# Kernel tuning notes

Measured on AMD Instinct MI355X. Metric: run time of the kernel, lower is better.

Reference implementation:

```python
import jax, jax.numpy as jnp
import numpy as np


def setup_inputs() -> dict:
    key = jax.random.key(0)
    ks = jax.random.split(key, 4)
    B, N, D, C = 8, 32768, 128, 64
    H = D // 2
    features = jax.random.normal(ks[0], (B, N, D), dtype=jnp.float32)
    cluster_assignments = jax.random.randint(ks[1], (B, N), 0, C)
    W1 = jax.random.normal(ks[2], (D, H), dtype=jnp.float32) * (1.0 / np.sqrt(D))
    b1 = jnp.zeros((H,), dtype=jnp.float32)
    W2 = jax.random.normal(ks[3], (H, 1), dtype=jnp.float32) * (1.0 / np.sqrt(H))
    b2 = jnp.zeros((1,), dtype=jnp.float32)
    return {"features": features, "cluster_assignments": cluster_assignments,
            "W1": W1, "b1": b1, "W2": W2, "b2": b2, "num_clusters": C}


def reference(features, cluster_assignments, W1, b1, W2, b2, num_clusters):
    # features: [B, N, D]; cluster_assignments: [B, N] ints in [0, num_clusters)
    B, N, D = features.shape
    # importance_net: Linear -> ReLU -> Linear -> Sigmoid
    h = jax.nn.relu(jnp.einsum('bnd,dh->bnh', features, W1) + b1)
    imp = jax.nn.sigmoid(jnp.einsum('bnh,ho->bno', h, W2) + b2)[..., 0]  # [B, N]

    # Fused per-(batch, cluster) softmax-weighted segment sum.
    num_seg = B * num_clusters
    seg = (cluster_assignments + num_clusters * jnp.arange(B)[:, None]).reshape(-1)  # [B*N]
    imp_f = imp.reshape(-1)
    # stable softmax within each segment
    seg_max = jax.ops.segment_max(imp_f, seg, num_segments=num_seg)  # -inf for empty
    e = jnp.exp(imp_f - seg_max[seg])
    denom = jax.ops.segment_sum(e, seg, num_segments=num_seg)
    w = e / denom[seg]  # [B*N]
    out = jax.ops.segment_sum(features.reshape(-1, D) * w[:, None], seg,
                              num_segments=num_seg)  # empty clusters -> zeros
    return out.reshape(B, num_clusters, D)
```

## Files before the change

### kernel.cpp

```cpp
#include <hip/hip_runtime.h>
#include <hip/hip_bf16.h>


#define B_ 8
#define N_ 32768
#define D_ 128
#define C_ 64
#define H_ 64

#define NTHREADS 512
#define NWAVES 8
#define ROWS_PER_BLOCK 512
#define NBLOCKS ((B_ * N_) / ROWS_PER_BLOCK)
#define SLICES (NBLOCKS / B_)
#define NSS 4
#define RST 152
#define W1S 136

typedef float f32x4 __attribute__((ext_vector_type(4)));
typedef short s16x8 __attribute__((ext_vector_type(8)));

__device__ __forceinline__ short bf16rne(float x) {
    unsigned u = __float_as_uint(x);
    u = (u + 0x7FFFu + ((u >> 16) & 1u)) >> 16;
    return (short)u;
}

__device__ __forceinline__ s16x8 pk8(float4 a, float4 b) {
    union { s16x8 v; __hip_bfloat162 h[4]; } u;
    u.h[0] = __float22bfloat162_rn(make_float2(a.x, a.y));
    u.h[1] = __float22bfloat162_rn(make_float2(a.z, a.w));
    u.h[2] = __float22bfloat162_rn(make_float2(b.x, b.y));
    u.h[3] = __float22bfloat162_rn(make_float2(b.z, b.w));
    return u.v;
}

template <bool USE_WS>
__global__ __launch_bounds__(NTHREADS, 4)
__attribute__((amdgpu_waves_per_eu(4, 4)))
void ca_fused_kernel(const float* __restrict__ features,
                     const int* __restrict__ ca,
                     const float* __restrict__ b1,
                     const float* __restrict__ W2,
                     const float* __restrict__ b2,
                     const float* __restrict__ W1,
                     float* __restrict__ out_sums,
                     float* __restrict__ denoms,
                     float* __restrict__ pout,
                     float* __restrict__ pden)
{
    __shared__ __align__(16) unsigned short ft[D_ * RST];
    __shared__ __align__(16) unsigned short w1l[H_ * W1S];
    __shared__ __align__(16) unsigned int ceu[128];

    const int tid  = threadIdx.x;
    const int lane = tid & 63;
    const int wave = tid >> 6;
    const int m    = lane & 15;
    const int kb   = lane >> 4;
    const int kbase = kb * 8;
    const int bidx = blockIdx.x;
    const int b    = bidx / SLICES;
    const int row_blk0 = bidx * ROWS_PER_BLOCK;

    for (int i = tid; i < H_ * D_; i += NTHREADS) {
        const int k = i >> 6, h = i & 63;
        w1l[h * W1S + k] = (unsigned short)bf16rne(W1[i]);
    }

    float b1v[4], w2v[4];
#pragma unroll
    for (int nt = 0; nt < 4; ++nt) {
        b1v[nt] = b1[nt * 16 + m];
        w2v[nt] = W2[nt * 16 + m];
    }
    const float b2v = b2[0];

    const int CH = wave >> 1;
    const int dh = wave & 1;

    f32x4 accS[4];
    f32x4 accD = (f32x4){0.f, 0.f, 0.f, 0.f};
#pragma unroll
    for (int nt = 0; nt < 4; ++nt) accS[nt] = (f32x4){0.f, 0.f, 0.f, 0.f};

    s16x8 bones;
    {
        const short o = (m == 0) ? (short)0x3F80 : (short)0;
#pragma unroll
        for (int j = 0; j < 8; ++j) bones[j] = o;
    }

    const float* fbase = features + (long long)(row_blk0 + wave * 16 + m) * D_;
    float4 pf[8];
#pragma unroll
    for (int ks = 0; ks < 4; ++ks) {
        pf[2 * ks]     = *(const float4*)(fbase + ks * 32 + kbase);
        pf[2 * ks + 1] = *(const float4*)(fbase + ks * 32 + kbase + 4);
    }
    int cv = 0;
    if (lane < 16) cv = ca[row_blk0 + wave * 16 + lane];

    __syncthreads();

#pragma unroll
    for (int ss = 0; ss < NSS; ++ss) {
        s16x8 af[4];
#pragma unroll
        for (int ks = 0; ks < 4; ++ks) af[ks] = pk8(pf[2 * ks], pf[2 * ks + 1]);
        const int cvc = cv;

        if (ss + 1 < NSS) {
            const float* fn = fbase + (ss + 1) * 128 * D_;
#pragma unroll
            for (int ks = 0; ks < 4; ++ks) {
                pf[2 * ks]     = *(const float4*)(fn + ks * 32 + kbase);
                pf[2 * ks + 1] = *(const float4*)(fn + ks * 32 + kbase + 4);
            }
            if (lane < 16) cv = ca[row_blk0 + (ss + 1) * 128 + wave * 16 + lane];
        }

        const int r = wave * 16 + m;
#pragma unroll
        for (int ks = 0; ks < 4; ++ks)
#pragma unroll
            for (int j = 0; j < 8; ++j)
                ft[(ks * 32 + kbase + j) * RST + r] = (unsigned short)af[ks][j];

        f32x4 hacc[4];
#pragma unroll
        for (int nt = 0; nt < 4; ++nt) hacc[nt] = (f32x4){0.f, 0.f, 0.f, 0.f};
#pragma unroll
        for (int ks = 0; ks < 4; ++ks)
#pragma unroll
            for (int nt = 0; nt < 4; ++nt) {
                const s16x8 w = *(const s16x8*)&w1l[(nt * 16 + m) * W1S +
                                                    ks * 32 + kbase];
                hacc[nt] = __builtin_amdgcn_mfma_f32_16x16x32_bf16(
                    af[ks], w, hacc[nt], 0, 0, 0);
            }

        float p[4];
#pragma unroll
        for (int rr = 0; rr < 4; ++rr) {
            float sv = 0.f;
#pragma unroll
            for (int nt = 0; nt < 4; ++nt)
                sv = fmaf(fmaxf(hacc[nt][rr] + b1v[nt], 0.f), w2v[nt], sv);
#pragma unroll
            for (int off = 1; off < 16; off <<= 1)
                sv += __shfl_xor(sv, off, 64);
            const float pre = sv + b2v;
            const float imp = 1.f / (1.f + __expf(-pre));
            p[rr] = __expf(imp - 1.f);
        }
        const int q = lane & 3;
        const float prov = (q == 0) ? p[0] : (q == 1) ? p[1] : (q == 2) ? p[2] : p[3];
        const int srcl = ((m >> 2) << 4) | (m & 3);
        const float eL = __shfl(prov, srcl, 64);
        if (lane < 16)
            ceu[wave * 16 + lane] =
                ((unsigned)(unsigned short)bf16rne(eL) << 16) | (unsigned)cvc;

        __syncthreads();

#pragma unroll
        for (int kg = 0; kg < 4; ++kg) {
            const uint4* cq = (const uint4*)&ceu[kg * 32 + kbase];
            const uint4 ua = cq[0], ub = cq[1];
            const unsigned uu[8] = {ua.x, ua.y, ua.z, ua.w, ub.x, ub.y, ub.z, ub.w};

            s16x8 afr;
#pragma unroll
            for (int j = 0; j < 8; ++j)
                afr[j] = ((int)(uu[j] & 0xFFu) == CH * 16 + m)
                             ? (short)(uu[j] >> 16) : (short)0;

#pragma unroll
            for (int nt = 0; nt < 4; ++nt) {
                const int d0 = (dh * 4 + nt) * 16 + m;
                const s16x8 bfv = *(const s16x8*)&ft[d0 * RST + kg * 32 + kbase];
                accS[nt] = __builtin_amdgcn_mfma_f32_16x16x32_bf16(
                    afr, bfv, accS[nt], 0, 0, 0);
            }
            if (dh == 0)
                accD = __builtin_amdgcn_mfma_f32_16x16x32_bf16(afr, bones, accD, 0, 0, 0);
        }
        __syncthreads();
    }

#pragma unroll
    for (int nt = 0; nt < 4; ++nt)
#pragma unroll
        for (int qq = 0; qq < 4; ++qq) {
            const int idx = (CH * 16 + kb * 4 + qq) * D_ + (dh * 4 + nt) * 16 + m;
            if (USE_WS) pout[(size_t)bidx * (C_ * D_) + idx] = accS[nt][qq];
            else atomicAdd(&out_sums[b * (C_ * D_) + idx], accS[nt][qq]);
        }
    if (dh == 0 && m == 0) {
#pragma unroll
        for (int qq = 0; qq < 4; ++qq) {
            const int c = CH * 16 + kb * 4 + qq;
            if (USE_WS) pden[bidx * C_ + c] = accD[qq];
            else atomicAdd(&denoms[b * C_ + c], accD[qq]);
        }
    }
}

__global__ __launch_bounds__(512)
void ca_reduce_kernel(const float* __restrict__ pout,
                      const float* __restrict__ pden,
                      float* __restrict__ out)
{
    __shared__ float red[512];
    __shared__ float dns;

    const int bc = blockIdx.x;
    const int b  = bc >> 6;
    const int c  = bc & (C_ - 1);
    const int t  = threadIdx.x;
    const int d  = t & 127;
    const int sg = t >> 7;

    const float* pb = pout + ((size_t)(b * SLICES + sg * 16)) * (C_ * D_)
                           + c * D_ + d;
    float s = 0.f;
#pragma unroll 4
    for (int i = 0; i < 16; ++i) s += pb[(size_t)i * (C_ * D_)];
    red[t] = s;

    float dnv = 0.f;
    if (t < SLICES) dnv = pden[(b * SLICES + t) * C_ + c];
    if (t < 64) {
#pragma unroll
        for (int off = 32; off > 0; off >>= 1) dnv += __shfl_xor(dnv, off, 64);
        if (t == 0) dns = dnv;
    }
    __syncthreads();

    if (t < 128) {
        const float tot = red[t] + red[t + 128] + red[t + 256] + red[t + 384];
        const float dn = dns;
        out[(size_t)bc * D_ + t] = (dn > 0.f) ? (tot / dn) : 0.f;
    }
}

__global__ void ca_zero_kernel(float* __restrict__ out_sums,
                               float* __restrict__ denoms)
{
    const int i = blockIdx.x * blockDim.x + threadIdx.x;
    if (i < B_ * C_ * D_) out_sums[i] = 0.f;
    if (i < B_ * C_)      denoms[i] = 0.f;
}

__global__ void ca_finalize_kernel(float* __restrict__ out_sums,
                                   const float* __restrict__ denoms)
{
    const int i = blockIdx.x * blockDim.x + threadIdx.x;
    if (i >= B_ * C_ * D_) return;
    const int bc = i >> 7;
    const float den = denoms[bc];
    const float v = out_sums[i];
    out_sums[i] = (den > 0.f) ? (v / den) : 0.f;
}

extern "C" void kernel_launch(void* const* d_in, const int* in_sizes, int n_in,
                              void* d_out, int out_size, void* d_ws, size_t ws_size,
                              hipStream_t stream) {
    const float* features = (const float*)d_in[0];
    const int*   ca       = (const int*)  d_in[1];
    const float* W1       = (const float*)d_in[2];
    const float* b1       = (const float*)d_in[3];
    const float* W2       = (const float*)d_in[4];
    const float* b2       = (const float*)d_in[5];

    float* out = (float*)d_out;

    float* pden = (float*)d_ws;
    float* pout = (float*)((char*)d_ws + 131072);
    const size_t need_full = 131072 + (size_t)NBLOCKS * C_ * D_ * 4;

    if (ws_size >= need_full) {
        ca_fused_kernel<true><<<NBLOCKS, NTHREADS, 0, stream>>>(
            features, ca, b1, W2, b2, W1, nullptr, nullptr, pout, pden);
        ca_reduce_kernel<<<B_ * C_, 512, 0, stream>>>(pout, pden, out);
    } else {
        ca_zero_kernel<<<(B_ * C_ * D_ + 255) / 256, 256, 0, stream>>>(out, pden);
        ca_fused_kernel<false><<<NBLOCKS, NTHREADS, 0, stream>>>(
            features, ca, b1, W2, b2, W1, out, pden, nullptr, nullptr);
        ca_finalize_kernel<<<(B_ * C_ * D_ + 255) / 256, 256, 0, stream>>>(out, pden);
    }
}
```

Before: 50.41 us.

## Halve block size to 256 rows and give each wave two cluster groups

Blocks shrink from 512 threads and 512 rows to 256 threads and 256 rows, which doubles the grid. Each of the 4 waves now accumulates two 16-cluster groups for its half of D, so every ft B-fragment load feeds two MFMAs. Every wave also computes the denominator for its own cluster group. The reduce kernel and workspace layout are updated for twice as many slices. The per-block partial output doubles the workspace writes and the reduce-kernel reads, and removing the waves_per_eu attribute changes register and occupancy behaviour.

```diff
diff --git a/kernel.cpp b/kernel.cpp
--- a/kernel.cpp
+++ b/kernel.cpp
@@ -8,13 +8,13 @@
 #define C_ 64
 #define H_ 64
 
-#define NTHREADS 512
-#define NWAVES 8
-#define ROWS_PER_BLOCK 512
+#define NTHREADS 256
+#define NWAVES 4
+#define ROWS_PER_BLOCK 256
 #define NBLOCKS ((B_ * N_) / ROWS_PER_BLOCK)
 #define SLICES (NBLOCKS / B_)
 #define NSS 4
-#define RST 152
+#define RST2 72
 #define W1S 136
 
 typedef float f32x4 __attribute__((ext_vector_type(4)));
@@ -37,7 +37,6 @@
 
 template <bool USE_WS>
 __global__ __launch_bounds__(NTHREADS, 4)
-__attribute__((amdgpu_waves_per_eu(4, 4)))
 void ca_fused_kernel(const float* __restrict__ features,
                      const int* __restrict__ ca,
                      const float* __restrict__ b1,
@@ -49,9 +48,9 @@
                      float* __restrict__ pout,
                      float* __restrict__ pden)
 {
-    __shared__ __align__(16) unsigned short ft[D_ * RST];
+    __shared__ __align__(16) unsigned short ft[D_ * RST2];
     __shared__ __align__(16) unsigned short w1l[H_ * W1S];
-    __shared__ __align__(16) unsigned int ceu[128];
+    __shared__ __align__(16) unsigned int ceu[64];
 
     const int tid  = threadIdx.x;
     const int lane = tid & 63;
@@ -76,13 +75,18 @@
     }
     const float b2v = b2[0];
 
-    const int CH = wave >> 1;
-    const int dh = wave & 1;
-
-    f32x4 accS[4];
+    const int CH2 = wave >> 1;
+    const int dh  = wave & 1;
+    const int c4a = CH2 * 2;
+    const int c4b = CH2 * 2 + 1;
+
+    f32x4 accSa[4], accSb[4];
     f32x4 accD = (f32x4){0.f, 0.f, 0.f, 0.f};
 #pragma unroll
-    for (int nt = 0; nt < 4; ++nt) accS[nt] = (f32x4){0.f, 0.f, 0.f, 0.f};
+    for (int nt = 0; nt < 4; ++nt) {
+        accSa[nt] = (f32x4){0.f, 0.f, 0.f, 0.f};
+        accSb[nt] = (f32x4){0.f, 0.f, 0.f, 0.f};
+    }
 
     s16x8 bones;
     {
@@ -111,13 +115,13 @@
         const int cvc = cv;
 
         if (ss + 1 < NSS) {
-            const float* fn = fbase + (ss + 1) * 128 * D_;
+            const float* fn = fbase + (ss + 1) * 64 * D_;
 #pragma unroll
             for (int ks = 0; ks < 4; ++ks) {
                 pf[2 * ks]     = *(const float4*)(fn + ks * 32 + kbase);
                 pf[2 * ks + 1] = *(const float4*)(fn + ks * 32 + kbase + 4);
             }
-            if (lane < 16) cv = ca[row_blk0 + (ss + 1) * 128 + wave * 16 + lane];
+            if (lane < 16) cv = ca[row_blk0 + (ss + 1) * 64 + wave * 16 + lane];
         }
 
         const int r = wave * 16 + m;
@@ -125,7 +129,7 @@
         for (int ks = 0; ks < 4; ++ks)
 #pragma unroll
             for (int j = 0; j < 8; ++j)
-                ft[(ks * 32 + kbase + j) * RST + r] = (unsigned short)af[ks][j];
+                ft[(ks * 32 + kbase + j) * RST2 + r] = (unsigned short)af[ks][j];
 
         f32x4 hacc[4];
 #pragma unroll
@@ -165,26 +169,31 @@
         __syncthreads();
 
 #pragma unroll
-        for (int kg = 0; kg < 4; ++kg) {
+        for (int kg = 0; kg < 2; ++kg) {
             const uint4* cq = (const uint4*)&ceu[kg * 32 + kbase];
             const uint4 ua = cq[0], ub = cq[1];
             const unsigned uu[8] = {ua.x, ua.y, ua.z, ua.w, ub.x, ub.y, ub.z, ub.w};
 
-            s16x8 afr;
-#pragma unroll
-            for (int j = 0; j < 8; ++j)
-                afr[j] = ((int)(uu[j] & 0xFFu) == CH * 16 + m)
-                             ? (short)(uu[j] >> 16) : (short)0;
+            s16x8 afrA, afrB;
+#pragma unroll
+            for (int j = 0; j < 8; ++j) {
+                const int cj = (int)(uu[j] & 0xFFu);
+                const short ej = (short)(uu[j] >> 16);
+                afrA[j] = (cj == c4a * 16 + m) ? ej : (short)0;
+                afrB[j] = (cj == c4b * 16 + m) ? ej : (short)0;
+            }
 
 #pragma unroll
             for (int nt = 0; nt < 4; ++nt) {
-                const int d0 = (dh * 4 + nt) * 16 + m;
-                const s16x8 bfv = *(const s16x8*)&ft[d0 * RST + kg * 32 + kbase];
-                accS[nt] = __builtin_amdgcn_mfma_f32_16x16x32_bf16(
-                    afr, bfv, accS[nt], 0, 0, 0);
-            }
-            if (dh == 0)
-                accD = __builtin_amdgcn_mfma_f32_16x16x32_bf16(afr, bones, accD, 0, 0, 0);
+                const int d0 = dh * 64 + nt * 16 + m;
+                const s16x8 bfv = *(const s16x8*)&ft[d0 * RST2 + kg * 32 + kbase];
+                accSa[nt] = __builtin_amdgcn_mfma_f32_16x16x32_bf16(
+                    afrA, bfv, accSa[nt], 0, 0, 0);
+                accSb[nt] = __builtin_amdgcn_mfma_f32_16x16x32_bf16(
+                    afrB, bfv, accSb[nt], 0, 0, 0);
+            }
+            accD = __builtin_amdgcn_mfma_f32_16x16x32_bf16(
+                (dh == 0) ? afrA : afrB, bones, accD, 0, 0, 0);
         }
         __syncthreads();
     }
@@ -193,14 +202,21 @@
     for (int nt = 0; nt < 4; ++nt)
 #pragma unroll
         for (int qq = 0; qq < 4; ++qq) {
-            const int idx = (CH * 16 + kb * 4 + qq) * D_ + (dh * 4 + nt) * 16 + m;
-            if (USE_WS) pout[(size_t)bidx * (C_ * D_) + idx] = accS[nt][qq];
-            else atomicAdd(&out_sums[b * (C_ * D_) + idx], accS[nt][qq]);
-        }
-    if (dh == 0 && m == 0) {
+            const int d0  = dh * 64 + nt * 16 + m;
+            const int ia = (c4a * 16 + kb * 4 + qq) * D_ + d0;
+            const int ib = (c4b * 16 + kb * 4 + qq) * D_ + d0;
+            if (USE_WS) {
+                pout[(size_t)bidx * (C_ * D_) + ia] = accSa[nt][qq];
+                pout[(size_t)bidx * (C_ * D_) + ib] = accSb[nt][qq];
+            } else {
+                atomicAdd(&out_sums[b * (C_ * D_) + ia], accSa[nt][qq]);
+                atomicAdd(&out_sums[b * (C_ * D_) + ib], accSb[nt][qq]);
+            }
+        }
+    if (m == 0) {
 #pragma unroll
         for (int qq = 0; qq < 4; ++qq) {
-            const int c = CH * 16 + kb * 4 + qq;
+            const int c = wave * 16 + kb * 4 + qq;
             if (USE_WS) pden[bidx * C_ + c] = accD[qq];
             else atomicAdd(&denoms[b * C_ + c], accD[qq]);
         }
@@ -213,7 +229,7 @@
                       float* __restrict__ out)
 {
     __shared__ float red[512];
-    __shared__ float dns;
+    __shared__ float redD[2];
 
     const int bc = blockIdx.x;
     const int b  = bc >> 6;
@@ -222,25 +238,24 @@
     const int d  = t & 127;
     const int sg = t >> 7;
 
-    const float* pb = pout + ((size_t)(b * SLICES + sg * 16)) * (C_ * D_)
+    const float* pb = pout + ((size_t)(b * SLICES + sg * 32)) * (C_ * D_)
                            + c * D_ + d;
     float s = 0.f;
 #pragma unroll 4
-    for (int i = 0; i < 16; ++i) s += pb[(size_t)i * (C_ * D_)];
+    for (int i = 0; i < 32; ++i) s += pb[(size_t)i * (C_ * D_)];
     red[t] = s;
 
-    float dnv = 0.f;
-    if (t < SLICES) dnv = pden[(b * SLICES + t) * C_ + c];
-    if (t < 64) {
+    if (t < 128) {
+        float dnv = pden[(b * SLICES + t) * C_ + c];
 #pragma unroll
         for (int off = 32; off > 0; off >>= 1) dnv += __shfl_xor(dnv, off, 64);
-        if (t == 0) dns = dnv;
+        if ((t & 63) == 0) redD[t >> 6] = dnv;
     }
     __syncthreads();
 
     if (t < 128) {
         const float tot = red[t] + red[t + 128] + red[t + 256] + red[t + 384];
-        const float dn = dns;
+        const float dn = redD[0] + redD[1];
         out[(size_t)bc * D_ + t] = (dn > 0.f) ? (tot / dn) : 0.f;
     }
 }
@@ -277,8 +292,9 @@
     float* out = (float*)d_out;
 
     float* pden = (float*)d_ws;
-    float* pout = (float*)((char*)d_ws + 131072);
-    const size_t need_full = 131072 + (size_t)NBLOCKS * C_ * D_ * 4;
+    float* pout = (float*)((char*)d_ws + (size_t)NBLOCKS * C_ * 4);
+    const size_t need_full =
+        (size_t)NBLOCKS * C_ * 4 + (size_t)NBLOCKS * C_ * D_ * 4;
 
     if (ws_size >= need_full) {
         ca_fused_kernel<true><<<NBLOCKS, NTHREADS, 0, stream>>>(
```

Measured after the change: 60.64 us. 1.2x slower.
